# Kernel tuning notes

Hardware: AMD Instinct MI355X
Metric: run time of the kernel (lower is better)

## Reference

```python
import jax, jax.numpy as jnp
import numpy as np

H, L, N = 1024, 2048, 32
EPS = 1e-7


def _hippo_lambda(n):
    # make_NPLR_HiPPO(2n) -> eigenvalues of skew part, keep first n with imag>0, shift by -0.5
    i = np.arange(2 * n, dtype=np.float64)
    x = 2 * i + 1
    hippo = np.tril(np.sqrt(np.outer(x, x)), k=-1)
    skew = (hippo - hippo.T) / 2
    lam = np.linalg.eig(skew)[0]
    idx = np.nonzero(lam.imag > 0)[0][:n]
    lam_sel = lam[idx] - 0.5
    return np.stack([lam_sel.real, lam_sel.imag], -1).astype(np.float32)


def setup_inputs() -> dict:
    key = jax.random.key(0)
    k1, k2, k3 = jax.random.split(key, 3)
    u = jax.random.normal(k1, (H, L), dtype=jnp.float32)
    # lecun-style scale for W (fan_in ~ N)
    W = jax.random.normal(k2, (H, N, 2), dtype=jnp.float32) / np.float32(np.sqrt(N))
    # log_step_initializer(dt_min=1e-3, dt_max=0.1)
    log_step = jax.random.uniform(k3, (H,), dtype=jnp.float32) * np.float32(np.log(0.1) - np.log(1e-3)) + np.float32(np.log(1e-3))
    Lambda_ri = jnp.asarray(_hippo_lambda(N))
    D = jnp.ones((H,), dtype=jnp.float32)
    return {"u": u, "W": W, "Lambda_ri": Lambda_ri, "log_step": log_step, "D": D}


def _complex_softmax(x):
    # softmax over complex vector, stabilized by the entry with max real part
    x2 = x - x[jnp.argmax(x.real)]
    e = jnp.exp(x2)
    s = jnp.sum(e)
    return e * (s.conj() / (s * s.conj() + EPS))


def _dss_kernel(Wc, Lam, step, length):
    # P: (N, L) complex; kernel = (W / Lambda) @ complex_softmax_rows(P)
    P = (step * Lam)[:, None] * jnp.arange(length)
    S = jax.vmap(_complex_softmax)(P)
    return ((Wc / Lam) @ S).real  # (L,)


def _fft_conv(u, K):
    # non-circular convolution via zero-padded rfft of length 2L
    n = u.shape[0]
    ud = jnp.fft.rfft(jnp.pad(u, (0, n)))
    Kd = jnp.fft.rfft(jnp.pad(K, (0, n)))
    return jnp.fft.irfft(ud * Kd)[:n]


def reference(u, W, Lambda_ri, log_step, D):
    Lam = Lambda_ri[:, 0] + 1j * Lambda_ri[:, 1]  # shared HiPPO eigenvalues (N,)
    Wc = W[..., 0] + 1j * W[..., 1]               # (H, N) complex
    step = jnp.exp(log_step)                      # (H,)

    def per_channel(u_h, W_h, step_h, D_h):
        K = _dss_kernel(W_h, Lam, step_h, u_h.shape[0])
        return _fft_conv(u_h, K) + D_h * u_h

    return jax.vmap(per_channel)(u, Wc, step, D)
```

## Files before the change

kernel.cpp:

```cpp
#include <hip/hip_runtime.h>
#include <math.h>


static constexpr int kH = 1024;
static constexpr int kL = 2048;
static constexpr int kN = 32;
static constexpr int kChunk = 32;
static constexpr int kWaves = 4;
static constexpr int kMpW = kN / kWaves;
static constexpr float kEps = 1e-7f;
static constexpr int kYStride = kL + (kL >> 5) + 1;

__global__ void dss_setup_kernel(const float* __restrict__ W,
                                 const float* __restrict__ Lambda_ri,
                                 const float* __restrict__ log_step,
                                 float* __restrict__ zc) {
    int idx = blockIdx.x * blockDim.x + threadIdx.x;
    if (idx >= kH * kN) return;
    int h = idx / kN;
    int n = idx % kN;

    float step = expf(log_step[h]);
    float lr = Lambda_ri[2 * n + 0];
    float li = Lambda_ri[2 * n + 1];
    float wr = W[(h * kN + n) * 2 + 0];
    float wi = W[(h * kN + n) * 2 + 1];

    float ar = step * lr;
    float ai = step * li;

    float ea = expf(ar);
    float sb, cb;
    sincosf(ai, &sb, &cb);

    float em = expm1f(ar);
    float sh = sinf(0.5f * ai);
    float dr = fmaf(-em, cb, 2.f * sh * sh);
    float di = -ea * sb;

    float eL = expf(ar * (float)kL);
    float sL, cL;
    sincosf(ai * (float)kL, &sL, &cL);
    float nr = 1.f - eL * cL;
    float ni = -eL * sL;

    float dd = dr * dr + di * di;
    float id = 1.f / dd;
    float sr = (nr * dr + ni * di) * id;
    float si = (ni * dr - nr * di) * id;

    float ll = lr * lr + li * li;
    float il = 1.f / ll;
    float qr = (wr * lr + wi * li) * il;
    float qi = (wi * lr - wr * li) * il;

    float ss = fmaf(sr, sr, fmaf(si, si, kEps));
    float is = 1.f / ss;

    float eC = expf(ar * (float)kChunk);
    float sC, cC;
    sincosf(ai * (float)kChunk, &sC, &cC);

    float* o = zc + (size_t)idx * 8;
    o[0] = ea * cb;              o[1] = ea * sb;
    o[2] = (qr * sr + qi * si) * is;
    o[3] = (qi * sr - qr * si) * is;
    o[4] = eC * cC;              o[5] = eC * sC;
    o[6] = 0.f;                  o[7] = 0.f;
}

__global__ __launch_bounds__(256, 4)
void dss_scan_kernel(const float* __restrict__ u,
                     const float* __restrict__ zc,
                     const float* __restrict__ Dv,
                     float* __restrict__ y) {
    __shared__ float y_s[kWaves][kYStride];

    const int h = blockIdx.x;
    const int tid = threadIdx.x;
    const int wave = tid >> 6;
    const int lane = tid & 63;

    const float4* uh4 = (const float4*)(u + (size_t)h * kL) + lane * 8;
    float uu[kChunk];
#pragma unroll
    for (int k = 0; k < 8; ++k) {
        const float4 v = uh4[k];
        uu[4 * k + 0] = v.x; uu[4 * k + 1] = v.y;
        uu[4 * k + 2] = v.z; uu[4 * k + 3] = v.w;
    }

    const int m0 = __builtin_amdgcn_readfirstlane((tid >> 6) * kMpW);
    const float* zch = zc + ((size_t)h * kN + m0) * 8;
    float zr[kMpW], zi[kMpW], cr[kMpW], ci[kMpW];
#pragma unroll
    for (int n = 0; n < kMpW; ++n) {
        zr[n] = zch[n * 8 + 0];
        zi[n] = zch[n * 8 + 1];
        cr[n] = zch[n * 8 + 2];
        ci[n] = zch[n * 8 + 3];
    }

    float er[kMpW], ei[kMpW];
#pragma unroll
    for (int n = 0; n < kMpW; ++n) { er[n] = 0.f; ei[n] = 0.f; }

#pragma unroll
    for (int k = 0; k < kChunk; ++k) {
        const float uv = uu[k];
#pragma unroll
        for (int n = 0; n < kMpW; ++n) {
            const float tr = zi[n] * er[n];
            er[n] = fmaf(zr[n], er[n], fmaf(-zi[n], ei[n], uv));
            ei[n] = fmaf(zr[n], ei[n], tr);
        }
    }

#pragma unroll
    for (int n = 0; n < kMpW; ++n) {
        const float vr = __shfl_up(er[n], 1);
        const float vi = __shfl_up(ei[n], 1);
        er[n] = (lane >= 1) ? vr : 0.f;
        ei[n] = (lane >= 1) ? vi : 0.f;
    }
    float pr[kMpW], pi[kMpW];
#pragma unroll
    for (int n = 0; n < kMpW; ++n) {
        pr[n] = zch[n * 8 + 4];
        pi[n] = zch[n * 8 + 5];
    }
#pragma unroll
    for (int d = 1; d < 64; d <<= 1) {
#pragma unroll
        for (int n = 0; n < kMpW; ++n) {
            float vr = __shfl_up(er[n], d);
            float vi = __shfl_up(ei[n], d);
            const bool ok = (lane >= d);
            vr = ok ? vr : 0.f;
            vi = ok ? vi : 0.f;
            er[n] = fmaf(pr[n], vr, fmaf(-pi[n], vi, er[n]));
            ei[n] = fmaf(pr[n], vi, fmaf(pi[n], vr, ei[n]));
        }
        if (d < 32) {
#pragma unroll
            for (int n = 0; n < kMpW; ++n) {
                const float t = fmaf(pr[n], pr[n], -pi[n] * pi[n]);
                pi[n] = 2.f * pr[n] * pi[n];
                pr[n] = t;
            }
        }
    }

    const float Dh = Dv[h];
    float* ys = &y_s[wave][0] + lane * 33;
#pragma unroll
    for (int k = 0; k < kChunk; ++k) {
        const float uv = uu[k];
        float acc = (wave == 0) ? Dh * uv : 0.f;
#pragma unroll
        for (int n = 0; n < kMpW; ++n) {
            const float tr = zi[n] * er[n];
            er[n] = fmaf(zr[n], er[n], fmaf(-zi[n], ei[n], uv));
            ei[n] = fmaf(zr[n], ei[n], tr);
            acc = fmaf(cr[n], er[n], acc);
            acc = fmaf(-ci[n], ei[n], acc);
        }
        ys[k] = acc;
    }
    __syncthreads();

    float* yh = y + (size_t)h * kL;
    for (int i = tid; i < kL; i += 256) {
        const int idx = i + (i >> 5);
        yh[i] = (y_s[0][idx] + y_s[1][idx]) + (y_s[2][idx] + y_s[3][idx]);
    }
}

extern "C" void kernel_launch(void* const* d_in, const int* in_sizes, int n_in,
                              void* d_out, int out_size, void* d_ws, size_t ws_size,
                              hipStream_t stream) {
    const float* u        = (const float*)d_in[0];
    const float* W        = (const float*)d_in[1];
    const float* Lam      = (const float*)d_in[2];
    const float* log_step = (const float*)d_in[3];
    const float* Dv       = (const float*)d_in[4];
    float* y  = (float*)d_out;
    float* zc = (float*)d_ws;

    dss_setup_kernel<<<(kH * kN + 255) / 256, 256, 0, stream>>>(W, Lam, log_step, zc);
    dss_scan_kernel<<<kH, 256, 0, stream>>>(u, zc, Dv, y);
}
```

Baseline: 90.62 us.

## Recast chunked diagonal SSM scan as bf16-split MFMA matrix products

The per-lane sequential complex recurrence over each 32-sample chunk is replaced by matrix products on MFMA units. Chunk-end states come from a Vandermonde-power matrix times the input chunk. The intra-chunk output comes from a Toeplitz kernel matrix plus a carry-readout matrix, all precomputed per channel in the setup kernel. FP32 precision is approximated by splitting operands into high and low bf16 parts across three MFMAs. The inter-chunk scan still uses shuffles. This removes the long serial FMA chains, at the cost of a heavier setup kernel, extra workspace tables, and reduced numerical precision.

```diff
diff --git a/kernel.cpp b/kernel.cpp
--- a/kernel.cpp
+++ b/kernel.cpp
@@ -5,174 +5,262 @@
 static constexpr int kH = 1024;
 static constexpr int kL = 2048;
 static constexpr int kN = 32;
-static constexpr int kChunk = 32;
-static constexpr int kWaves = 4;
-static constexpr int kMpW = kN / kWaves;
 static constexpr float kEps = 1e-7f;
-static constexpr int kYStride = kL + (kL >> 5) + 1;
-
-__global__ void dss_setup_kernel(const float* __restrict__ W,
-                                 const float* __restrict__ Lambda_ri,
-                                 const float* __restrict__ log_step,
-                                 float* __restrict__ zc) {
-    int idx = blockIdx.x * blockDim.x + threadIdx.x;
-    if (idx >= kH * kN) return;
-    int h = idx / kN;
-    int n = idx % kN;
-
-    float step = expf(log_step[h]);
-    float lr = Lambda_ri[2 * n + 0];
-    float li = Lambda_ri[2 * n + 1];
-    float wr = W[(h * kN + n) * 2 + 0];
-    float wi = W[(h * kN + n) * 2 + 1];
-
-    float ar = step * lr;
-    float ai = step * li;
-
-    float ea = expf(ar);
-    float sb, cb;
-    sincosf(ai, &sb, &cb);
-
-    float em = expm1f(ar);
-    float sh = sinf(0.5f * ai);
-    float dr = fmaf(-em, cb, 2.f * sh * sh);
-    float di = -ea * sb;
-
-    float eL = expf(ar * (float)kL);
-    float sL, cL;
-    sincosf(ai * (float)kL, &sL, &cL);
-    float nr = 1.f - eL * cL;
-    float ni = -eL * sL;
-
-    float dd = dr * dr + di * di;
-    float id = 1.f / dd;
-    float sr = (nr * dr + ni * di) * id;
-    float si = (ni * dr - nr * di) * id;
-
-    float ll = lr * lr + li * li;
-    float il = 1.f / ll;
-    float qr = (wr * lr + wi * li) * il;
-    float qi = (wi * lr - wr * li) * il;
-
-    float ss = fmaf(sr, sr, fmaf(si, si, kEps));
-    float is = 1.f / ss;
-
-    float eC = expf(ar * (float)kChunk);
-    float sC, cC;
-    sincosf(ai * (float)kChunk, &sC, &cC);
-
-    float* o = zc + (size_t)idx * 8;
-    o[0] = ea * cb;              o[1] = ea * sb;
-    o[2] = (qr * sr + qi * si) * is;
-    o[3] = (qi * sr - qr * si) * is;
-    o[4] = eC * cC;              o[5] = eC * sC;
-    o[6] = 0.f;                  o[7] = 0.f;
-}
-
-__global__ __launch_bounds__(256, 4)
-void dss_scan_kernel(const float* __restrict__ u,
-                     const float* __restrict__ zc,
-                     const float* __restrict__ Dv,
-                     float* __restrict__ y) {
-    __shared__ float y_s[kWaves][kYStride];
-
+
+typedef __attribute__((ext_vector_type(8))) short s8;
+typedef __attribute__((ext_vector_type(4))) float f4;
+
+__device__ __forceinline__ unsigned short f2bf(float x) {
+    union { float f; unsigned u; } v; v.f = x;
+    return (unsigned short)((v.u + 0x7fffu + ((v.u >> 16) & 1u)) >> 16);
+}
+__device__ __forceinline__ float bf2f(unsigned short b) {
+    union { unsigned u; float f; } v; v.u = ((unsigned)b) << 16; return v.f;
+}
+__device__ __forceinline__ size_t TBL(int t, int h, int q, int lane) {
+    return ((((size_t)t * kH + h) * 2 + q) * 64 + (size_t)lane) * 8;
+}
+
+__global__ void dss_setup(const float* __restrict__ W,
+                          const float* __restrict__ Lam,
+                          const float* __restrict__ logstep,
+                          float* __restrict__ zc,
+                          unsigned short* __restrict__ fb) {
+    __shared__ float K_s[8][32];
+    __shared__ float zc_s[8][32][4];
+    const int tid = threadIdx.x;
+    const int chl = tid >> 5;
+    const int h = blockIdx.x * 8 + chl;
+    const int n = tid & 31;
+    K_s[chl][n] = 0.f;
+    __syncthreads();
+
+    float step = expf(logstep[h]);
+    float lr = Lam[2*n], li = Lam[2*n+1];
+    float wr = W[((size_t)h*kN+n)*2], wi = W[((size_t)h*kN+n)*2+1];
+    float ar = step*lr, ai = step*li;
+    float ea = expf(ar); float sb, cb; sincosf(ai, &sb, &cb);
+    float zr = ea*cb, zi = ea*sb;
+    float em = expm1f(ar); float shh = sinf(0.5f*ai);
+    float dr = fmaf(-em, cb, 2.f*shh*shh), di = -ea*sb;
+    float eL = expf(ar*(float)kL); float sL, cL; sincosf(ai*(float)kL, &sL, &cL);
+    float nr = 1.f - eL*cL, ni = -eL*sL;
+    float dd = dr*dr + di*di, id = 1.f/dd;
+    float sr = (nr*dr + ni*di)*id, si = (ni*dr - nr*di)*id;
+    float ll = lr*lr + li*li, il = 1.f/ll;
+    float qr = (wr*lr + wi*li)*il, qi = (wi*lr - wr*li)*il;
+    float ssq = fmaf(sr,sr, fmaf(si,si,kEps)); float is = 1.f/ssq;
+    float cr = (qr*sr + qi*si)*is, ci = (qi*sr - qr*si)*is;
+
+    s8 zrh[4], zrl[4], zih[4], zil[4];
+    float pr = 1.f, pi = 0.f;
+#pragma unroll
+    for (int e = 0; e < 32; ++e) {
+        const int k = 31 - e, g = k >> 3, j = k & 7;
+        unsigned short hr = f2bf(pr);
+        zrh[g][j] = (short)hr; zrl[g][j] = (short)f2bf(pr - bf2f(hr));
+        unsigned short hi_ = f2bf(pi);
+        zih[g][j] = (short)hi_; zil[g][j] = (short)f2bf(pi - bf2f(hi_));
+        atomicAdd(&K_s[chl][e], fmaf(cr, pr, -ci*pi));
+        float t = fmaf(pr, zr, -pi*zi);
+        pi = fmaf(pr, zi, pi*zr);
+        pr = t;
+    }
+    float* o = zc + ((size_t)h*kN + n)*8;
+    o[0]=zr; o[1]=zi; o[2]=cr; o[3]=ci; o[4]=pr; o[5]=pi; o[6]=0.f; o[7]=0.f;
+    zc_s[chl][n][0]=zr; zc_s[chl][n][1]=zi; zc_s[chl][n][2]=cr; zc_s[chl][n][3]=ci;
+    {
+        const int mb = n >> 4, rl = n & 15;
+#pragma unroll
+        for (int g = 0; g < 4; ++g) {
+            *(s8*)(fb + TBL(0,h,mb,rl+16*g)) = zrh[g];
+            *(s8*)(fb + TBL(1,h,mb,rl+16*g)) = zrl[g];
+            *(s8*)(fb + TBL(2,h,mb,rl+16*g)) = zih[g];
+            *(s8*)(fb + TBL(3,h,mb,rl+16*g)) = zil[g];
+        }
+    }
+    __syncthreads();
+
+    const int i = n;
+    s8 rrh[4], rrl[4], rnh[4], rnl[4];
+#pragma unroll
+    for (int m = 0; m < 32; ++m) {
+        const float bzr = zc_s[chl][m][0], bzi = zc_s[chl][m][1];
+        const float bcr = zc_s[chl][m][2], bci = zc_s[chl][m][3];
+        float ppr = 1.f, ppi = 0.f, br = bzr, bi = bzi;
+        const int e = i + 1;
+#pragma unroll
+        for (int b = 0; b < 6; ++b) {
+            if ((e >> b) & 1) {
+                float t = fmaf(ppr, br, -ppi*bi);
+                ppi = fmaf(ppr, bi, ppi*br); ppr = t;
+            }
+            float t2 = fmaf(br, br, -bi*bi); bi = 2.f*br*bi; br = t2;
+        }
+        const float Rre = fmaf(bcr, ppr, -bci*ppi);
+        const float Rni = -fmaf(bcr, ppi, bci*ppr);
+        const int g = m >> 3, j = m & 7;
+        unsigned short h1 = f2bf(Rre); rrh[g][j] = (short)h1; rrl[g][j] = (short)f2bf(Rre - bf2f(h1));
+        unsigned short h2 = f2bf(Rni); rnh[g][j] = (short)h2; rnl[g][j] = (short)f2bf(Rni - bf2f(h2));
+    }
+    const int ib = i >> 4, rl2 = i & 15;
+#pragma unroll
+    for (int g = 0; g < 4; ++g) {
+        *(s8*)(fb + TBL(4,h,ib,rl2+16*g)) = rrh[g];
+        *(s8*)(fb + TBL(5,h,ib,rl2+16*g)) = rrl[g];
+        *(s8*)(fb + TBL(6,h,ib,rl2+16*g)) = rnh[g];
+        *(s8*)(fb + TBL(7,h,ib,rl2+16*g)) = rnl[g];
+    }
+    s8 th[4], tl[4];
+#pragma unroll
+    for (int j = 0; j < 32; ++j) {
+        const float kv = (j <= i) ? K_s[chl][i - j] : 0.f;
+        unsigned short hv = f2bf(kv);
+        th[j>>3][j&7] = (short)hv; tl[j>>3][j&7] = (short)f2bf(kv - bf2f(hv));
+    }
+#pragma unroll
+    for (int g = 0; g < 4; ++g) {
+        *(s8*)(fb + TBL(8,h,ib,rl2+16*g)) = th[g];
+        *(s8*)(fb + TBL(9,h,ib,rl2+16*g)) = tl[g];
+    }
+}
+
+__global__ __launch_bounds__(256)
+void dss_main(const float* __restrict__ u,
+              const float* __restrict__ zc,
+              const unsigned short* __restrict__ fb,
+              const float* __restrict__ Dv,
+              float* __restrict__ y) {
+    __shared__ float SL[64][66];
+    __shared__ float CarL[64][68];
     const int h = blockIdx.x;
     const int tid = threadIdx.x;
-    const int wave = tid >> 6;
+    const int wv = tid >> 6;
     const int lane = tid & 63;
-
-    const float4* uh4 = (const float4*)(u + (size_t)h * kL) + lane * 8;
-    float uu[kChunk];
-#pragma unroll
-    for (int k = 0; k < 8; ++k) {
-        const float4 v = uh4[k];
-        uu[4 * k + 0] = v.x; uu[4 * k + 1] = v.y;
-        uu[4 * k + 2] = v.z; uu[4 * k + 3] = v.w;
-    }
-
-    const int m0 = __builtin_amdgcn_readfirstlane((tid >> 6) * kMpW);
-    const float* zch = zc + ((size_t)h * kN + m0) * 8;
-    float zr[kMpW], zi[kMpW], cr[kMpW], ci[kMpW];
-#pragma unroll
-    for (int n = 0; n < kMpW; ++n) {
-        zr[n] = zch[n * 8 + 0];
-        zi[n] = zch[n * 8 + 1];
-        cr[n] = zch[n * 8 + 2];
-        ci[n] = zch[n * 8 + 3];
-    }
-
-    float er[kMpW], ei[kMpW];
-#pragma unroll
-    for (int n = 0; n < kMpW; ++n) { er[n] = 0.f; ei[n] = 0.f; }
-
-#pragma unroll
-    for (int k = 0; k < kChunk; ++k) {
-        const float uv = uu[k];
-#pragma unroll
-        for (int n = 0; n < kMpW; ++n) {
-            const float tr = zi[n] * er[n];
-            er[n] = fmaf(zr[n], er[n], fmaf(-zi[n], ei[n], uv));
-            ei[n] = fmaf(zr[n], ei[n], tr);
-        }
-    }
-
-#pragma unroll
-    for (int n = 0; n < kMpW; ++n) {
-        const float vr = __shfl_up(er[n], 1);
-        const float vi = __shfl_up(ei[n], 1);
-        er[n] = (lane >= 1) ? vr : 0.f;
-        ei[n] = (lane >= 1) ? vi : 0.f;
-    }
-    float pr[kMpW], pi[kMpW];
-#pragma unroll
-    for (int n = 0; n < kMpW; ++n) {
-        pr[n] = zch[n * 8 + 4];
-        pi[n] = zch[n * 8 + 5];
-    }
-#pragma unroll
+    const int cl = lane & 15;
+    const int hq = lane >> 4;
+    const int c = 16*wv + cl;
+
+    const float* ug = u + (size_t)h*kL;
+    float uu[8];
+    {
+        const f4 a0 = *(const f4*)(ug + 32*c + 8*hq);
+        const f4 a1 = *(const f4*)(ug + 32*c + 8*hq + 4);
+        uu[0]=a0.x; uu[1]=a0.y; uu[2]=a0.z; uu[3]=a0.w;
+        uu[4]=a1.x; uu[5]=a1.y; uu[6]=a1.z; uu[7]=a1.w;
+    }
+    s8 Uh, Ul;
+#pragma unroll
+    for (int j = 0; j < 8; ++j) {
+        unsigned short hv = f2bf(uu[j]);
+        Uh[j] = (short)hv; Ul[j] = (short)f2bf(uu[j] - bf2f(hv));
+    }
+
+    f4 Sre[2] = {{0.f,0.f,0.f,0.f},{0.f,0.f,0.f,0.f}};
+    f4 Sim[2] = {{0.f,0.f,0.f,0.f},{0.f,0.f,0.f,0.f}};
+#pragma unroll
+    for (int mb = 0; mb < 2; ++mb) {
+        s8 a0 = *(const s8*)(fb + TBL(0,h,mb,lane));
+        s8 a1 = *(const s8*)(fb + TBL(1,h,mb,lane));
+        s8 a2 = *(const s8*)(fb + TBL(2,h,mb,lane));
+        s8 a3 = *(const s8*)(fb + TBL(3,h,mb,lane));
+        Sre[mb] = __builtin_amdgcn_mfma_f32_16x16x32_bf16(a0, Uh, Sre[mb], 0,0,0);
+        Sre[mb] = __builtin_amdgcn_mfma_f32_16x16x32_bf16(a0, Ul, Sre[mb], 0,0,0);
+        Sre[mb] = __builtin_amdgcn_mfma_f32_16x16x32_bf16(a1, Uh, Sre[mb], 0,0,0);
+        Sim[mb] = __builtin_amdgcn_mfma_f32_16x16x32_bf16(a2, Uh, Sim[mb], 0,0,0);
+        Sim[mb] = __builtin_amdgcn_mfma_f32_16x16x32_bf16(a2, Ul, Sim[mb], 0,0,0);
+        Sim[mb] = __builtin_amdgcn_mfma_f32_16x16x32_bf16(a3, Uh, Sim[mb], 0,0,0);
+    }
+#pragma unroll
+    for (int mb = 0; mb < 2; ++mb)
+#pragma unroll
+        for (int r = 0; r < 4; ++r) {
+            const int mode = 16*mb + 4*hq + r;
+            *(float2*)&SL[c][2*mode] = make_float2(Sre[mb][r], Sim[mb][r]);
+        }
+    __syncthreads();
+
+    float Xr[8], Xi[8];
+#pragma unroll
+    for (int q = 0; q < 8; ++q) {
+        float2 v = *(const float2*)&SL[lane][16*wv + 2*q];
+        Xr[q] = v.x; Xi[q] = v.y;
+    }
+#pragma unroll
+    for (int q = 0; q < 8; ++q) {
+        float vr = __shfl_up(Xr[q], 1), vi = __shfl_up(Xi[q], 1);
+        Xr[q] = (lane >= 1) ? vr : 0.f;
+        Xi[q] = (lane >= 1) ? vi : 0.f;
+    }
+    const int wvu = __builtin_amdgcn_readfirstlane(wv);
+    const float* zch = zc + ((size_t)h*kN + 8*wvu)*8;
+    float pr[8], pi[8];
+#pragma unroll
+    for (int q = 0; q < 8; ++q) { pr[q] = zch[q*8+4]; pi[q] = zch[q*8+5]; }
+#pragma unroll 1
     for (int d = 1; d < 64; d <<= 1) {
 #pragma unroll
-        for (int n = 0; n < kMpW; ++n) {
-            float vr = __shfl_up(er[n], d);
-            float vi = __shfl_up(ei[n], d);
-            const bool ok = (lane >= d);
-            vr = ok ? vr : 0.f;
-            vi = ok ? vi : 0.f;
-            er[n] = fmaf(pr[n], vr, fmaf(-pi[n], vi, er[n]));
-            ei[n] = fmaf(pr[n], vi, fmaf(pi[n], vr, ei[n]));
-        }
-        if (d < 32) {
-#pragma unroll
-            for (int n = 0; n < kMpW; ++n) {
-                const float t = fmaf(pr[n], pr[n], -pi[n] * pi[n]);
-                pi[n] = 2.f * pr[n] * pi[n];
-                pr[n] = t;
-            }
-        }
-    }
+        for (int q = 0; q < 8; ++q) {
+            float vr = __shfl_up(Xr[q], d), vi = __shfl_up(Xi[q], d);
+            const bool ok = lane >= d;
+            vr = ok ? vr : 0.f; vi = ok ? vi : 0.f;
+            Xr[q] = fmaf(pr[q], vr, fmaf(-pi[q], vi, Xr[q]));
+            Xi[q] = fmaf(pr[q], vi, fmaf(pi[q], vr, Xi[q]));
+        }
+#pragma unroll
+        for (int q = 0; q < 8; ++q) {
+            float t = fmaf(pr[q], pr[q], -pi[q]*pi[q]);
+            pi[q] = 2.f*pr[q]*pi[q]; pr[q] = t;
+        }
+    }
+#pragma unroll
+    for (int v2 = 0; v2 < 4; ++v2) {
+        *(f4*)&CarL[lane][16*wvu + 4*v2] =
+            (f4){Xr[2*v2], Xi[2*v2], Xr[2*v2+1], Xi[2*v2+1]};
+    }
+    __syncthreads();
+
+    s8 Crh, Crl, Cih, Cil;
+#pragma unroll
+    for (int v2 = 0; v2 < 4; ++v2) {
+        const f4 cv = *(const f4*)&CarL[c][16*hq + 4*v2];
+        unsigned short t1 = f2bf(cv.x); Crh[2*v2]   = (short)t1; Crl[2*v2]   = (short)f2bf(cv.x - bf2f(t1));
+        unsigned short t2 = f2bf(cv.z); Crh[2*v2+1] = (short)t2; Crl[2*v2+1] = (short)f2bf(cv.z - bf2f(t2));
+        unsigned short t3 = f2bf(cv.y); Cih[2*v2]   = (short)t3; Cil[2*v2]   = (short)f2bf(cv.y - bf2f(t3));
+        unsigned short t4 = f2bf(cv.w); Cih[2*v2+1] = (short)t4; Cil[2*v2+1] = (short)f2bf(cv.w - bf2f(t4));
+    }
+    f4 acc[2] = {{0.f,0.f,0.f,0.f},{0.f,0.f,0.f,0.f}};
+#pragma unroll
+    for (int ib = 0; ib < 2; ++ib) {
+        s8 t0 = *(const s8*)(fb + TBL(8,h,ib,lane));
+        s8 t1 = *(const s8*)(fb + TBL(9,h,ib,lane));
+        acc[ib] = __builtin_amdgcn_mfma_f32_16x16x32_bf16(t0, Uh, acc[ib], 0,0,0);
+        acc[ib] = __builtin_amdgcn_mfma_f32_16x16x32_bf16(t0, Ul, acc[ib], 0,0,0);
+        acc[ib] = __builtin_amdgcn_mfma_f32_16x16x32_bf16(t1, Uh, acc[ib], 0,0,0);
+        s8 r0 = *(const s8*)(fb + TBL(4,h,ib,lane));
+        s8 r1 = *(const s8*)(fb + TBL(5,h,ib,lane));
+        s8 r2 = *(const s8*)(fb + TBL(6,h,ib,lane));
+        s8 r3 = *(const s8*)(fb + TBL(7,h,ib,lane));
+        acc[ib] = __builtin_amdgcn_mfma_f32_16x16x32_bf16(r0, Crh, acc[ib], 0,0,0);
+        acc[ib] = __builtin_amdgcn_mfma_f32_16x16x32_bf16(r0, Crl, acc[ib], 0,0,0);
+        acc[ib] = __builtin_amdgcn_mfma_f32_16x16x32_bf16(r1, Crh, acc[ib], 0,0,0);
+        acc[ib] = __builtin_amdgcn_mfma_f32_16x16x32_bf16(r2, Cih, acc[ib], 0,0,0);
+        acc[ib] = __builtin_amdgcn_mfma_f32_16x16x32_bf16(r2, Cil, acc[ib], 0,0,0);
+        acc[ib] = __builtin_amdgcn_mfma_f32_16x16x32_bf16(r3, Cih, acc[ib], 0,0,0);
+    }
+    float* yl = &SL[0][0];
+#pragma unroll
+    for (int ib = 0; ib < 2; ++ib)
+#pragma unroll
+        for (int r = 0; r < 4; ++r) {
+            yl[c*34 + 16*ib + 4*hq + r] = acc[ib][r];
+        }
+    __syncthreads();
 
     const float Dh = Dv[h];
-    float* ys = &y_s[wave][0] + lane * 33;
-#pragma unroll
-    for (int k = 0; k < kChunk; ++k) {
-        const float uv = uu[k];
-        float acc = (wave == 0) ? Dh * uv : 0.f;
-#pragma unroll
-        for (int n = 0; n < kMpW; ++n) {
-            const float tr = zi[n] * er[n];
-            er[n] = fmaf(zr[n], er[n], fmaf(-zi[n], ei[n], uv));
-            ei[n] = fmaf(zr[n], ei[n], tr);
-            acc = fmaf(cr[n], er[n], acc);
-            acc = fmaf(-ci[n], ei[n], acc);
-        }
-        ys[k] = acc;
-    }
-    __syncthreads();
-
-    float* yh = y + (size_t)h * kL;
-    for (int i = tid; i < kL; i += 256) {
-        const int idx = i + (i >> 5);
-        yh[i] = (y_s[0][idx] + y_s[1][idx]) + (y_s[2][idx] + y_s[3][idx]);
+    float* yg = y + (size_t)h*kL;
+    for (int e = tid; e < kL; e += 256) {
+        yg[e] = fmaf(Dh, ug[e], yl[(e >> 5)*34 + (e & 31)]);
     }
 }
 
@@ -186,7 +274,8 @@
     const float* Dv       = (const float*)d_in[4];
     float* y  = (float*)d_out;
     float* zc = (float*)d_ws;
-
-    dss_setup_kernel<<<(kH * kN + 255) / 256, 256, 0, stream>>>(W, Lam, log_step, zc);
-    dss_scan_kernel<<<kH, 256, 0, stream>>>(u, zc, Dv, y);
-}
+    unsigned short* fb = (unsigned short*)(zc + (size_t)kH*kN*8);
+
+    dss_setup<<<kH/8, 256, 0, stream>>>(W, Lam, log_step, zc, fb);
+    dss_main<<<kH, 256, 0, stream>>>(u, zc, fb, Dv, y);
+}
```

Measured after the change: 102.2 us. +12.8%, slower.
